# Kernel optimization log

Measured on AMD Instinct MI355X. Metric: run time of the kernel, lower is better.

## Reference

```python
import jax, jax.numpy as jnp
import numpy as np

NUM_HEAD = 8
LN_EPS = 1e-5


def setup_inputs() -> dict:
    key = jax.random.key(0)
    ks = jax.random.split(key, 10)
    Nd = 32768          # num destination nodes
    E = 524288          # num edges (= num extra src nodes, TGL convention)
    Dn, De, Dt, Do = 128, 128, 128, 128

    h = jax.random.normal(ks[0], (Nd + E, Dn), dtype=jnp.float32)
    f = jax.random.normal(ks[1], (E, De), dtype=jnp.float32)
    dt = jax.random.uniform(ks[2], (E,), dtype=jnp.float32) * 100.0
    dst_idx = jax.random.randint(ks[3], (E,), 0, Nd, dtype=jnp.int32)

    # TimeEncode params (init = 1/10^linspace(0,9,dim), bias 0; both learnable)
    freq = jnp.asarray(1.0 / 10.0 ** np.linspace(0, 9, Dt, dtype=np.float32))
    time_bias = jnp.zeros((Dt,), dtype=jnp.float32)

    def lin(k, out_d, in_d):
        s = 1.0 / np.sqrt(in_d)
        return jax.random.uniform(k, (out_d, in_d), jnp.float32, -s, s)

    Wq = lin(ks[4], Do, Dn + Dt)
    Wk = lin(ks[5], Do, Dn + De + Dt)
    Wv = lin(ks[6], Do, Dn + De + Dt)
    Wout = lin(ks[7], Do, Dn + Do)
    bq = jnp.zeros((Do,), jnp.float32)
    bk = jnp.zeros((Do,), jnp.float32)
    bv = jnp.zeros((Do,), jnp.float32)
    bout = jnp.zeros((Do,), jnp.float32)
    ln_gamma = jnp.ones((Do,), jnp.float32)
    ln_beta = jnp.zeros((Do,), jnp.float32)

    return {"h": h, "f": f, "dt": dt, "dst_idx": dst_idx,
            "freq": freq, "time_bias": time_bias,
            "Wq": Wq, "bq": bq, "Wk": Wk, "bk": bk, "Wv": Wv, "bv": bv,
            "Wout": Wout, "bout": bout, "ln_gamma": ln_gamma, "ln_beta": ln_beta}


def reference(h, f, dt, dst_idx, freq, time_bias, Wq, bq, Wk, bk, Wv, bv,
              Wout, bout, ln_gamma, ln_beta):
    E = dt.shape[0]
    Nd = h.shape[0] - E          # srcdata['h'][:Nd] are dst nodes, rest map 1:1 to edges
    Do = Wq.shape[0]
    H = NUM_HEAD

    h_dst = h[:Nd]               # [Nd, Dn]
    h_src = h[Nd:]               # [E, Dn], source node of edge i is Nd+i

    # TimeEncode: cos(t * freq + bias)
    time_feat = jnp.cos(dt[:, None] * freq[None, :] + time_bias)      # [E, Dt]
    zero_time_feat = jnp.broadcast_to(jnp.cos(time_bias), (Nd, freq.shape[0]))

    # Q over dst nodes, gathered per edge
    Q_in = jnp.concatenate([h_dst, zero_time_feat], axis=1)           # [Nd, Dn+Dt]
    Q_nodes = Q_in @ Wq.T + bq                                        # [Nd, Do]
    Q = Q_nodes[dst_idx]                                              # [E, Do]

    # K/V over per-edge (src node, edge feat, time feat)
    KV_in = jnp.concatenate([h_src, f, time_feat], axis=1)            # [E, Dn+De+Dt]
    K = KV_in @ Wk.T + bk
    V = KV_in @ Wv.T + bv

    Qh = Q.reshape(E, H, -1)
    Kh = K.reshape(E, H, -1)
    Vh = V.reshape(E, H, -1)

    logits = jax.nn.leaky_relu(jnp.sum(Qh * Kh, axis=2), 0.2)         # [E, H]

    # edge_softmax: softmax over edges sharing the same destination node
    seg_max = jax.ops.segment_max(logits, dst_idx, num_segments=Nd)   # [Nd, H]
    ex = jnp.exp(logits - seg_max[dst_idx])
    seg_sum = jax.ops.segment_sum(ex, dst_idx, num_segments=Nd)       # [Nd, H]
    att = ex / seg_sum[dst_idx]                                       # [E, H]

    Vw = (Vh * att[:, :, None]).reshape(E, Do)                        # [E, Do]
    agg = jax.ops.segment_sum(Vw, dst_idx, num_segments=Nd)           # [Nd, Do]

    rst = jnp.concatenate([agg, h_dst], axis=1) @ Wout.T + bout       # [Nd, Do]
    rst = jax.nn.relu(rst)                                            # dropout=0 (eval)

    mu = jnp.mean(rst, axis=-1, keepdims=True)
    var = jnp.var(rst, axis=-1, keepdims=True)
    return (rst - mu) / jnp.sqrt(var + LN_EPS) * ln_gamma + ln_beta
```

## Files before the change

kernel.cpp:

```cpp
#include <hip/hip_runtime.h>
#include <hip/hip_bf16.h>
#include <cstdint>
#include <cstddef>

#define LN_EPS 1e-5f

typedef __attribute__((ext_vector_type(8))) short short8;
typedef __attribute__((ext_vector_type(4))) float f32x4;

static __device__ __forceinline__ unsigned short f2bf(float x) {
    union { float f; unsigned u; } v; v.f = x;
    unsigned r = v.u + 0x7FFFu + ((v.u >> 16) & 1u);
    return (unsigned short)(r >> 16);
}
static __device__ __forceinline__ float bf2f(unsigned short b) {
    union { unsigned u; float f; } v; v.u = ((unsigned)b) << 16;
    return v.f;
}
static __device__ __forceinline__ unsigned cvt2(float lo, float hi) {
    float2 p; p.x = lo; p.y = hi;
    __hip_bfloat162 h = __float22bfloat162_rn(p);
    unsigned u; __builtin_memcpy(&u, &h, 4); return u;
}

__global__ void prep_kernel(const float* __restrict__ Wq, const float* __restrict__ bq,
                            const float* __restrict__ Wk, const float* __restrict__ Wv,
                            const float* __restrict__ Wout, const float* __restrict__ tb,
                            unsigned short* __restrict__ wkv, unsigned short* __restrict__ wq,
                            unsigned short* __restrict__ wout, float* __restrict__ qbias) {
    int tid = blockIdx.x * blockDim.x + threadIdx.x;
    if (tid < 256 * 384) {
        int o = tid / 384, k = tid % 384;
        float w = (o < 128) ? Wk[o * 384 + k] : Wv[(o - 128) * 384 + k];
        wkv[tid] = f2bf(w);
    }
    if (tid < 128 * 128) {
        int o = tid / 128, i = tid % 128;
        wq[tid] = f2bf(Wq[o * 256 + i]);
    }
    if (tid < 128 * 256) {
        wout[tid] = f2bf(Wout[tid]);
    }
    if (tid < 128) {
        float s = bq[tid];
        for (int t = 0; t < 128; ++t) s += cosf(tb[t]) * Wq[tid * 256 + 128 + t];
        qbias[tid] = s;
    }
}

__launch_bounds__(512, 4)
__global__ void gemm_kv_kernel(const float* __restrict__ h, const float* __restrict__ f,
                               const float* __restrict__ dt, const float* __restrict__ freq,
                               const float* __restrict__ tb,
                               const unsigned short* __restrict__ wkv,
                               const float* __restrict__ bk, const float* __restrict__ bv,
                               unsigned short* __restrict__ Kb, unsigned short* __restrict__ Vb,
                               int Nd, int E) {
    __shared__ __align__(1024) float ldsA[2][8192];
    const int tid = threadIdx.x;
    const int w  = tid >> 6, l = tid & 63, ln = l & 15, lq = l >> 4;
    const int wm = w >> 2, wn = w & 3;
    const long e_base = (long)blockIdx.x * 128;

    auto stage = [&](int c, int buf) {
        #pragma unroll
        for (int i = 0; i < 4; ++i) {
            int inst = w * 4 + i;
            int a    = inst * 1024 + l * 16;
            int row  = a >> 8;
            int colb = (a & 255) ^ ((row & 7) << 5);
            long er  = e_base + row; if (er >= E) er = E - 1;
            const float* g = (c < 2) ? h + ((long)Nd + er) * 128 + c * 64 + (colb >> 2)
                                     : f + er * 128 + (c - 2) * 64 + (colb >> 2);
            __builtin_amdgcn_global_load_lds(
                (const __attribute__((address_space(1))) void*)g,
                (__attribute__((address_space(3))) void*)&ldsA[buf][inst * 256],
                16, 0, 0);
        }
    };

    stage(0, 0);
    f32x4 acc[4][4] = {};
    __syncthreads();

    int buf = 0;
    #pragma unroll
    for (int c = 0; c < 4; ++c) {
        short8 wfr[2][4];
        #pragma unroll
        for (int ksl = 0; ksl < 2; ++ksl)
            #pragma unroll
            for (int nt = 0; nt < 4; ++nt) {
                int o = wn * 64 + nt * 16 + ln;
                wfr[ksl][nt] = *(const short8*)(wkv + o * 384 + c * 64 + ksl * 32 + lq * 8);
            }
        if (c < 3) stage(c + 1, buf ^ 1);
        #pragma unroll
        for (int ksl = 0; ksl < 2; ++ksl) {
            #pragma unroll
            for (int mt = 0; mt < 4; ++mt) {
                int row = wm * 64 + mt * 16 + ln;
                int swz = ((ksl * 32 + lq * 8) << 2) ^ ((row & 7) << 5);
                const float* p = &ldsA[buf][row * 64 + (swz >> 2)];
                float4 x0 = *(const float4*)p;
                float4 x1 = *(const float4*)(p + 4);
                union { short8 s; unsigned u[4]; } v;
                v.u[0] = cvt2(x0.x, x0.y); v.u[1] = cvt2(x0.z, x0.w);
                v.u[2] = cvt2(x1.x, x1.y); v.u[3] = cvt2(x1.z, x1.w);
                #pragma unroll
                for (int nt = 0; nt < 4; ++nt)
                    acc[mt][nt] = __builtin_amdgcn_mfma_f32_16x16x32_bf16(
                        wfr[ksl][nt], v.s, acc[mt][nt], 0, 0, 0);
            }
        }
        __syncthreads();
        buf ^= 1;
    }

    float dval[4];
    #pragma unroll
    for (int mt = 0; mt < 4; ++mt) {
        long e = e_base + wm * 64 + mt * 16 + ln;
        if (e >= E) e = E - 1;
        dval[mt] = dt[e];
    }
    #pragma unroll
    for (int ks = 0; ks < 4; ++ks) {
        int t0 = ks * 32 + lq * 8;
        short8 wfr[4];
        #pragma unroll
        for (int nt = 0; nt < 4; ++nt) {
            int o = wn * 64 + nt * 16 + ln;
            wfr[nt] = *(const short8*)(wkv + o * 384 + 256 + ks * 32 + lq * 8);
        }
        float4 f0 = *(const float4*)(freq + t0);
        float4 f1 = *(const float4*)(freq + t0 + 4);
        float4 b0 = *(const float4*)(tb + t0);
        float4 b1 = *(const float4*)(tb + t0 + 4);
        #pragma unroll
        for (int mt = 0; mt < 4; ++mt) {
            float d = dval[mt];
            union { short8 s; unsigned u[4]; } v;
            v.u[0] = cvt2(__cosf(fmaf(d, f0.x, b0.x)), __cosf(fmaf(d, f0.y, b0.y)));
            v.u[1] = cvt2(__cosf(fmaf(d, f0.z, b0.z)), __cosf(fmaf(d, f0.w, b0.w)));
            v.u[2] = cvt2(__cosf(fmaf(d, f1.x, b1.x)), __cosf(fmaf(d, f1.y, b1.y)));
            v.u[3] = cvt2(__cosf(fmaf(d, f1.z, b1.z)), __cosf(fmaf(d, f1.w, b1.w)));
            #pragma unroll
            for (int nt = 0; nt < 4; ++nt)
                acc[mt][nt] = __builtin_amdgcn_mfma_f32_16x16x32_bf16(
                    wfr[nt], v.s, acc[mt][nt], 0, 0, 0);
        }
    }

    #pragma unroll
    for (int nt = 0; nt < 4; ++nt) {
        int o0 = wn * 64 + nt * 16 + lq * 4;
        const float* bsrc = (o0 < 128) ? (bk + o0) : (bv + (o0 - 128));
        float4 b4 = *(const float4*)bsrc;
        #pragma unroll
        for (int mt = 0; mt < 4; ++mt) {
            long e = e_base + wm * 64 + mt * 16 + ln;
            if (e >= E) continue;
            f32x4 a = acc[mt][nt];
            uint2 u;
            u.x = cvt2(a[0] + b4.x, a[1] + b4.y);
            u.y = cvt2(a[2] + b4.z, a[3] + b4.w);
            unsigned short* dst = (o0 < 128) ? (Kb + e * 128 + o0)
                                             : (Vb + e * 128 + (o0 - 128));
            *(uint2*)dst = u;
        }
    }
}

__launch_bounds__(256)
__global__ void gemm_node_kernel(const float* __restrict__ src0, const float* __restrict__ src1,
                                 const unsigned short* __restrict__ W, const float* __restrict__ bias,
                                 float* __restrict__ out, int M, int ksteps, int do_relu) {
    __shared__ unsigned short ldsA[4 * 8 * 64 * 8];
    const int tid = threadIdx.x;
    const long m_base = (long)blockIdx.x * 64;
    const int Kd = ksteps * 32;
    const int g4 = Kd / 4;

    for (int g = tid; g < 64 * g4; g += 256) {
        int r  = g / g4;
        int c4 = (g % g4) * 4;
        long m = m_base + r; if (m >= M) m = M - 1;
        float4 x = (c4 < 128) ? *(const float4*)(src0 + m * 128 + c4)
                              : *(const float4*)(src1 + m * 128 + (c4 - 128));
        int lane = (r & 15) | (((c4 >> 3) & 3) << 4);
        int base = (((r >> 4) * ksteps + (c4 >> 5)) * 64 + lane) * 8 + (c4 & 7);
        *(unsigned*)&ldsA[base]     = cvt2(x.x, x.y);
        *(unsigned*)&ldsA[base + 2] = cvt2(x.z, x.w);
    }
    __syncthreads();

    const int w = tid >> 6, l = tid & 63, ln = l & 15, lq = l >> 4;
    f32x4 acc[4][2] = {};
    for (int ks = 0; ks < ksteps; ++ks) {
        short8 bfr[2];
        #pragma unroll
        for (int nt = 0; nt < 2; ++nt) {
            int row = w * 32 + nt * 16 + ln;
            bfr[nt] = *(const short8*)(W + row * Kd + ks * 32 + lq * 8);
        }
        #pragma unroll
        for (int mt = 0; mt < 4; ++mt) {
            short8 afr = *(const short8*)&ldsA[((mt * ksteps + ks) * 64 + l) * 8];
            #pragma unroll
            for (int nt = 0; nt < 2; ++nt)
                acc[mt][nt] = __builtin_amdgcn_mfma_f32_16x16x32_bf16(
                    bfr[nt], afr, acc[mt][nt], 0, 0, 0);
        }
    }
    #pragma unroll
    for (int nt = 0; nt < 2; ++nt) {
        int o0 = w * 32 + nt * 16 + lq * 4;
        float4 b4 = *(const float4*)(bias + o0);
        #pragma unroll
        for (int mt = 0; mt < 4; ++mt) {
            long m = m_base + mt * 16 + ln;
            if (m >= M) continue;
            f32x4 a = acc[mt][nt];
            float4 o;
            o.x = a[0] + b4.x; o.y = a[1] + b4.y;
            o.z = a[2] + b4.z; o.w = a[3] + b4.w;
            if (do_relu) {
                o.x = fmaxf(o.x, 0.f); o.y = fmaxf(o.y, 0.f);
                o.z = fmaxf(o.z, 0.f); o.w = fmaxf(o.w, 0.f);
            }
            *(float4*)(out + m * 128 + o0) = o;
        }
    }
}

__global__ void hist_kernel(const int* __restrict__ dst, int* __restrict__ counts, int E) {
    int e = blockIdx.x * blockDim.x + threadIdx.x;
    if (e < E) atomicAdd(&counts[dst[e]], 1);
}

__global__ void scan_kernel(const int* __restrict__ counts, int* __restrict__ offsets,
                            int* __restrict__ cursor, int Nd) {
    __shared__ int sdata[1024];
    int t = threadIdx.x;
    int C = (Nd + 1023) / 1024;
    int b0 = t * C;
    int s = 0;
    for (int i = 0; i < C; ++i) { int idx = b0 + i; if (idx < Nd) s += counts[idx]; }
    sdata[t] = s;
    __syncthreads();
    for (int off = 1; off < 1024; off <<= 1) {
        int v = (t >= off) ? sdata[t - off] : 0;
        __syncthreads();
        sdata[t] += v;
        __syncthreads();
    }
    int run = sdata[t] - s;
    for (int i = 0; i < C; ++i) {
        int idx = b0 + i;
        if (idx < Nd) { offsets[idx] = run; cursor[idx] = run; run += counts[idx]; }
    }
}

__global__ void scatter_kernel(const int* __restrict__ dst, int* __restrict__ cursor,
                               int* __restrict__ order, int E) {
    int e = blockIdx.x * blockDim.x + threadIdx.x;
    if (e < E) { int pos = atomicAdd(&cursor[dst[e]], 1); order[pos] = e; }
}

__launch_bounds__(128)
__global__ void attn_kernel(const float* __restrict__ Q, const unsigned short* __restrict__ Kb,
                            const unsigned short* __restrict__ Vb,
                            const int* __restrict__ order, const int* __restrict__ offsets,
                            const int* __restrict__ counts, float* __restrict__ agg) {
    const int d = blockIdx.x;
    const int t = threadIdx.x;
    const int beg = offsets[d];
    const int n   = counts[d];
    const float q = Q[(long)d * 128 + t];

    float m = -3.0e38f, lsum = 0.f, acc = 0.f;
    float kk = 0.f, vv = 0.f;
    if (n > 0) {
        int e0 = order[beg];
        kk = bf2f(Kb[(long)e0 * 128 + t]);
        vv = bf2f(Vb[(long)e0 * 128 + t]);
    }
    for (int i = 0; i < n; ++i) {
        float ck = kk, cv = vv;
        if (i + 1 < n) {
            int e2 = order[beg + i + 1];
            kk = bf2f(Kb[(long)e2 * 128 + t]);
            vv = bf2f(Vb[(long)e2 * 128 + t]);
        }
        float p = q * ck;
        p += __shfl_xor(p, 1, 16);
        p += __shfl_xor(p, 2, 16);
        p += __shfl_xor(p, 4, 16);
        p += __shfl_xor(p, 8, 16);
        float logit = (p > 0.f) ? p : 0.2f * p;
        float mn = fmaxf(m, logit);
        float sc = __expf(m - mn);
        float pe = __expf(logit - mn);
        lsum = lsum * sc + pe;
        acc  = acc * sc + pe * cv;
        m = mn;
    }
    agg[(long)d * 128 + t] = (n > 0) ? acc / lsum : 0.f;
}

__launch_bounds__(256)
__global__ void ln_kernel(const float* __restrict__ rst, const float* __restrict__ gamma,
                          const float* __restrict__ beta, float* __restrict__ out, int Nd) {
    int wave = threadIdx.x >> 6;
    int lane = threadIdx.x & 63;
    long row = (long)blockIdx.x * 4 + wave;
    if (row >= Nd) return;
    float x0 = rst[row * 128 + lane];
    float x1 = rst[row * 128 + 64 + lane];
    float s = x0 + x1, sq = x0 * x0 + x1 * x1;
    #pragma unroll
    for (int off = 32; off >= 1; off >>= 1) {
        s  += __shfl_xor(s, off, 64);
        sq += __shfl_xor(sq, off, 64);
    }
    float mean = s * (1.f / 128.f);
    float var  = sq * (1.f / 128.f) - mean * mean;
    float rstd = rsqrtf(var + LN_EPS);
    out[row * 128 + lane]      = (x0 - mean) * rstd * gamma[lane]      + beta[lane];
    out[row * 128 + 64 + lane] = (x1 - mean) * rstd * gamma[lane + 64] + beta[lane + 64];
}

extern "C" void kernel_launch(void* const* d_in, const int* in_sizes, int n_in,
                              void* d_out, int out_size, void* d_ws, size_t ws_size,
                              hipStream_t stream) {
    const float* h    = (const float*)d_in[0];
    const float* f    = (const float*)d_in[1];
    const float* dt   = (const float*)d_in[2];
    const int*   dst  = (const int*)d_in[3];
    const float* freq = (const float*)d_in[4];
    const float* tb   = (const float*)d_in[5];
    const float* Wq   = (const float*)d_in[6];
    const float* bq   = (const float*)d_in[7];
    const float* Wk   = (const float*)d_in[8];
    const float* bk   = (const float*)d_in[9];
    const float* Wv   = (const float*)d_in[10];
    const float* bv   = (const float*)d_in[11];
    const float* Wout = (const float*)d_in[12];
    const float* bout = (const float*)d_in[13];
    const float* gamma= (const float*)d_in[14];
    const float* beta = (const float*)d_in[15];

    const int E  = in_sizes[2];
    const int Nd = in_sizes[0] / 128 - E;

    char* ws = (char*)d_ws;
    size_t off = 0;
    auto alloc = [&](size_t b) {
        off = (off + 255) & ~(size_t)255;
        char* p = ws + off; off += b; return p;
    };
    unsigned short* wkv   = (unsigned short*)alloc(256 * 384 * 2);
    unsigned short* wq    = (unsigned short*)alloc(128 * 128 * 2);
    unsigned short* wout  = (unsigned short*)alloc(128 * 256 * 2);
    float*          qbias = (float*)alloc(128 * 4);
    float*          Q     = (float*)alloc((size_t)Nd * 128 * 4);
    unsigned short* Kb    = (unsigned short*)alloc((size_t)E * 128 * 2);
    unsigned short* Vb    = (unsigned short*)alloc((size_t)E * 128 * 2);
    float*          agg   = (float*)alloc((size_t)Nd * 128 * 4);
    int*            counts= (int*)alloc((size_t)Nd * 4);
    int*            offs  = (int*)alloc((size_t)Nd * 4);
    int*            cursor= (int*)alloc((size_t)Nd * 4);
    int*            order = (int*)alloc((size_t)E * 4);
    float*          rst   = (float*)Kb;

    hipMemsetAsync(counts, 0, (size_t)Nd * 4, stream);
    prep_kernel<<<(256 * 384 + 255) / 256, 256, 0, stream>>>(Wq, bq, Wk, Wv, Wout, tb,
                                                             wkv, wq, wout, qbias);
    hist_kernel<<<(E + 255) / 256, 256, 0, stream>>>(dst, counts, E);
    scan_kernel<<<1, 1024, 0, stream>>>(counts, offs, cursor, Nd);
    scatter_kernel<<<(E + 255) / 256, 256, 0, stream>>>(dst, cursor, order, E);
    gemm_node_kernel<<<(Nd + 63) / 64, 256, 0, stream>>>(h, nullptr, wq, qbias, Q, Nd, 4, 0);
    gemm_kv_kernel<<<(E + 127) / 128, 512, 0, stream>>>(h, f, dt, freq, tb, wkv, bk, bv,
                                                        Kb, Vb, Nd, E);
    attn_kernel<<<Nd, 128, 0, stream>>>(Q, Kb, Vb, order, offs, counts, agg);
    gemm_node_kernel<<<(Nd + 63) / 64, 256, 0, stream>>>(agg, h, wout, bout, rst, Nd, 8, 1);
    ln_kernel<<<(Nd + 3) / 4, 256, 0, stream>>>(rst, gamma, beta, (float*)d_out, Nd);
}
```

Before: 1.208 ms.

## Stage KV GEMM outputs through LDS, retune swizzle, one wave per node in attention

The KV GEMM epilogue now writes bf16 results into LDS with an XOR swizzle and then stores them to global memory as 16-byte coalesced rows, replacing scattered 8-byte stores. The LDS A-tile swizzle moves from 32-byte granularity over 8 rows to 16-byte granularity over 16 rows, to reduce bank conflicts on the float4 reads. The attention kernel maps one 64-lane wave to each destination node, with each lane handling two bf16 elements via 32-bit loads and an 8-lane shuffle reduction per head, which raises occupancy and halves shuffle work. This adds an extra LDS round trip and a barrier at the end of the GEMM.

```diff
diff --git a/kernel.cpp b/kernel.cpp
--- a/kernel.cpp
+++ b/kernel.cpp
@@ -68,7 +68,7 @@
             int inst = w * 4 + i;
             int a    = inst * 1024 + l * 16;
             int row  = a >> 8;
-            int colb = (a & 255) ^ ((row & 7) << 5);
+            int colb = (a & 255) ^ ((row & 15) << 4);
             long er  = e_base + row; if (er >= E) er = E - 1;
             const float* g = (c < 2) ? h + ((long)Nd + er) * 128 + c * 64 + (colb >> 2)
                                      : f + er * 128 + (c - 2) * 64 + (colb >> 2);
@@ -100,10 +100,11 @@
             #pragma unroll
             for (int mt = 0; mt < 4; ++mt) {
                 int row = wm * 64 + mt * 16 + ln;
-                int swz = ((ksl * 32 + lq * 8) << 2) ^ ((row & 7) << 5);
-                const float* p = &ldsA[buf][row * 64 + (swz >> 2)];
-                float4 x0 = *(const float4*)p;
-                float4 x1 = *(const float4*)(p + 4);
+                int swz = (row & 15) << 4;
+                int c0  = ksl * 128 + lq * 32;
+                const char* base = (const char*)&ldsA[buf][0] + row * 256;
+                float4 x0 = *(const float4*)(base + ((c0     ) ^ swz));
+                float4 x1 = *(const float4*)(base + ((c0 + 16) ^ swz));
                 union { short8 s; unsigned u[4]; } v;
                 v.u[0] = cvt2(x0.x, x0.y); v.u[1] = cvt2(x0.z, x0.w);
                 v.u[2] = cvt2(x1.x, x1.y); v.u[3] = cvt2(x1.z, x1.w);
@@ -152,6 +153,7 @@
         }
     }
 
+    unsigned short* lout = (unsigned short*)&ldsA[0][0];
     #pragma unroll
     for (int nt = 0; nt < 4; ++nt) {
         int o0 = wn * 64 + nt * 16 + lq * 4;
@@ -159,15 +161,27 @@
         float4 b4 = *(const float4*)bsrc;
         #pragma unroll
         for (int mt = 0; mt < 4; ++mt) {
-            long e = e_base + wm * 64 + mt * 16 + ln;
-            if (e >= E) continue;
+            int el = wm * 64 + mt * 16 + ln;
             f32x4 a = acc[mt][nt];
             uint2 u;
             u.x = cvt2(a[0] + b4.x, a[1] + b4.y);
             u.y = cvt2(a[2] + b4.z, a[3] + b4.w);
-            unsigned short* dst = (o0 < 128) ? (Kb + e * 128 + o0)
-                                             : (Vb + e * 128 + (o0 - 128));
-            *(uint2*)dst = u;
+            int byte = (o0 * 2) ^ ((el & 7) << 4);
+            *(uint2*)((char*)lout + el * 512 + byte) = u;
+        }
+    }
+    __syncthreads();
+    #pragma unroll
+    for (int p = 0; p < 8; ++p) {
+        int g   = p * 512 + tid;
+        int el  = g >> 5;
+        int c16 = g & 31;
+        int byte = (c16 * 16) ^ ((el & 7) << 4);
+        uint4 dta = *(const uint4*)((const char*)lout + el * 512 + byte);
+        long e = e_base + el;
+        if (e < E) {
+            if (c16 < 16) *(uint4*)(Kb + e * 128 + c16 * 8) = dta;
+            else          *(uint4*)(Vb + e * 128 + (c16 - 16) * 8) = dta;
         }
     }
 }
@@ -268,45 +282,54 @@
     if (e < E) { int pos = atomicAdd(&cursor[dst[e]], 1); order[pos] = e; }
 }
 
-__launch_bounds__(128)
+__launch_bounds__(256)
 __global__ void attn_kernel(const float* __restrict__ Q, const unsigned short* __restrict__ Kb,
                             const unsigned short* __restrict__ Vb,
                             const int* __restrict__ order, const int* __restrict__ offsets,
-                            const int* __restrict__ counts, float* __restrict__ agg) {
-    const int d = blockIdx.x;
-    const int t = threadIdx.x;
+                            const int* __restrict__ counts, float* __restrict__ agg, int Nd) {
+    const int wv = threadIdx.x >> 6;
+    const int l  = threadIdx.x & 63;
+    const long d = (long)blockIdx.x * 4 + wv;
+    if (d >= Nd) return;
     const int beg = offsets[d];
     const int n   = counts[d];
-    const float q = Q[(long)d * 128 + t];
-
-    float m = -3.0e38f, lsum = 0.f, acc = 0.f;
-    float kk = 0.f, vv = 0.f;
+    float2 q = *(const float2*)(Q + d * 128 + l * 2);
+
+    float m = -3.0e38f, lsum = 0.f;
+    float2 acc; acc.x = 0.f; acc.y = 0.f;
+    unsigned kk = 0, vv = 0;
     if (n > 0) {
-        int e0 = order[beg];
-        kk = bf2f(Kb[(long)e0 * 128 + t]);
-        vv = bf2f(Vb[(long)e0 * 128 + t]);
+        long e0 = order[beg];
+        kk = *(const unsigned*)(Kb + e0 * 128 + l * 2);
+        vv = *(const unsigned*)(Vb + e0 * 128 + l * 2);
     }
     for (int i = 0; i < n; ++i) {
-        float ck = kk, cv = vv;
+        unsigned ck = kk, cv = vv;
         if (i + 1 < n) {
-            int e2 = order[beg + i + 1];
-            kk = bf2f(Kb[(long)e2 * 128 + t]);
-            vv = bf2f(Vb[(long)e2 * 128 + t]);
-        }
-        float p = q * ck;
-        p += __shfl_xor(p, 1, 16);
-        p += __shfl_xor(p, 2, 16);
-        p += __shfl_xor(p, 4, 16);
-        p += __shfl_xor(p, 8, 16);
+            long e2 = order[beg + i + 1];
+            kk = *(const unsigned*)(Kb + e2 * 128 + l * 2);
+            vv = *(const unsigned*)(Vb + e2 * 128 + l * 2);
+        }
+        float k0 = bf2f((unsigned short)(ck & 0xFFFFu));
+        float k1 = bf2f((unsigned short)(ck >> 16));
+        float p = q.x * k0 + q.y * k1;
+        p += __shfl_xor(p, 1, 8);
+        p += __shfl_xor(p, 2, 8);
+        p += __shfl_xor(p, 4, 8);
         float logit = (p > 0.f) ? p : 0.2f * p;
         float mn = fmaxf(m, logit);
         float sc = __expf(m - mn);
         float pe = __expf(logit - mn);
-        lsum = lsum * sc + pe;
-        acc  = acc * sc + pe * cv;
+        float v0 = bf2f((unsigned short)(cv & 0xFFFFu));
+        float v1 = bf2f((unsigned short)(cv >> 16));
+        lsum  = lsum  * sc + pe;
+        acc.x = acc.x * sc + pe * v0;
+        acc.y = acc.y * sc + pe * v1;
         m = mn;
     }
-    agg[(long)d * 128 + t] = (n > 0) ? acc / lsum : 0.f;
+    float inv = (n > 0) ? 1.f / lsum : 0.f;
+    float2 o; o.x = acc.x * inv; o.y = acc.y * inv;
+    *(float2*)(agg + d * 128 + l * 2) = o;
 }
 
 __launch_bounds__(256)
@@ -383,7 +406,7 @@
     gemm_node_kernel<<<(Nd + 63) / 64, 256, 0, stream>>>(h, nullptr, wq, qbias, Q, Nd, 4, 0);
     gemm_kv_kernel<<<(E + 127) / 128, 512, 0, stream>>>(h, f, dt, freq, tb, wkv, bk, bv,
                                                         Kb, Vb, Nd, E);
-    attn_kernel<<<Nd, 128, 0, stream>>>(Q, Kb, Vb, order, offs, counts, agg);
+    attn_kernel<<<(Nd + 3) / 4, 256, 0, stream>>>(Q, Kb, Vb, order, offs, counts, agg, Nd);
     gemm_node_kernel<<<(Nd + 63) / 64, 256, 0, stream>>>(agg, h, wout, bout, rst, Nd, 8, 1);
     ln_kernel<<<(Nd + 3) / 4, 256, 0, stream>>>(rst, gamma, beta, (float*)d_out, Nd);
 }
```

After: 1.151 ms. -4.7%, faster.
